# Kernel tuning notes

Measured on AMD Instinct MI355X. Metric: run time of the kernel, lower is better.

## Reference

```python
import jax, jax.numpy as jnp
import numpy as np

D_MODEL = 2048
NUM_EXPERTS = 64
TOP_K = 2


def setup_inputs() -> dict:
    key = jax.random.key(0)
    k_x, k_w = jax.random.split(key)
    x = jax.random.normal(k_x, (4, 8192, D_MODEL), dtype=jnp.float32)
    # nn.Linear(d_model, num_experts, bias=False): weight [num_experts, d_model]
    bound = 1.0 / np.sqrt(D_MODEL)
    W = jax.random.uniform(k_w, (NUM_EXPERTS, D_MODEL), dtype=jnp.float32,
                           minval=-bound, maxval=bound)
    return {"x": x, "W": W}


def reference(x, W):
    # router_logits = x @ W.T : [b, s, num_experts]
    logits = jnp.einsum("bsd,ed->bse", x, W)
    probs = jax.nn.softmax(logits, axis=-1)
    gates, indices = jax.lax.top_k(probs, TOP_K)  # [b, s, top_k]
    gates = gates / jnp.sum(gates, axis=-1, keepdims=True)
    return gates, indices
```

## Files before the change

kernel.cpp:

```cpp
#include <hip/hip_runtime.h>
#include <math.h>
#include <stdint.h>

#define D_MODEL 2048
#define NEXP    64
#define TOKENS  32768
#define BM      128
#define BK      32
#define NT      512
#define NCHUNK  (D_MODEL / BK)
#define BUFSZ   24576
#define TIE_THR 1e-3f
#define LSTRIDE 66

typedef __attribute__((ext_vector_type(8))) short short8;
typedef __attribute__((ext_vector_type(4))) float f32x4;
typedef __attribute__((ext_vector_type(4))) int   i32x4;

typedef __attribute__((address_space(3))) uint32_t       lds_u32_t;
typedef const __attribute__((address_space(1))) uint32_t gbl_u32_t;

__device__ __forceinline__ void split2(float f0, float f1, uint32_t& hw, uint32_t& lw)
{
    const uint32_t u0 = __float_as_uint(f0), u1 = __float_as_uint(f1);
    const uint32_t a0 = u0 & 0xffff0000u, a1 = u1 & 0xffff0000u;
    hw = a1 | (u0 >> 16);
    const float l0 = f0 - __uint_as_float(a0);
    const float l1 = f1 - __uint_as_float(a1);
    lw = (__float_as_uint(l1) & 0xffff0000u) | (__float_as_uint(l0) >> 16);
}

__device__ __forceinline__ void ldsplit(const char* p0, const char* p1,
                                        short8& h8, short8& l8)
{
    const float4 qa = *(const float4*)p0;
    const float4 qb = *(const float4*)p1;
    i32x4 hv, lv;
    uint32_t hw, lw;
    split2(qa.x, qa.y, hw, lw); hv[0] = (int)hw; lv[0] = (int)lw;
    split2(qa.z, qa.w, hw, lw); hv[1] = (int)hw; lv[1] = (int)lw;
    split2(qb.x, qb.y, hw, lw); hv[2] = (int)hw; lv[2] = (int)lw;
    split2(qb.z, qb.w, hw, lw); hv[3] = (int)hw; lv[3] = (int)lw;
    h8 = *(short8*)&hv;
    l8 = *(short8*)&lv;
}

#define WAITVM(N) asm volatile("s_waitcnt vmcnt(" #N ")" ::: "memory")

#define STAGE(c, b)                                                              \
    do {                                                                         \
        char* bb_ = smem + (b) * BUFSZ;                                          \
        __builtin_amdgcn_global_load_lds((gbl_u32_t*)(xsrc0 + (size_t)(c) * BK), \
            (lds_u32_t*)(bb_ + 2048 * wave), 16, 0, 0);                          \
        __builtin_amdgcn_global_load_lds((gbl_u32_t*)(xsrc1 + (size_t)(c) * BK), \
            (lds_u32_t*)(bb_ + 2048 * wave + 1024), 16, 0, 0);                   \
        __builtin_amdgcn_global_load_lds((gbl_u32_t*)(wsrc0 + (size_t)(c) * BK), \
            (lds_u32_t*)(bb_ + 16384 + 1024 * wave), 16, 0, 0);                  \
    } while (0)

#define COMPUTE(b)                                                               \
    do {                                                                         \
        const char* xb_ = smem + (b) * BUFSZ;                                    \
        const char* wb_ = xb_ + 16384;                                           \
        short8 ah_[2], al_[2], bh_[2], bl_[2];                                   \
        _Pragma("unroll")                                                        \
        for (int mi = 0; mi < 2; ++mi)                                           \
            ldsplit(xb_ + oA[mi], xb_ + (oA[mi] ^ 16), ah_[mi], al_[mi]);        \
        _Pragma("unroll")                                                        \
        for (int ni = 0; ni < 2; ++ni)                                           \
            ldsplit(wb_ + oB[ni], wb_ + (oB[ni] ^ 16), bh_[ni], bl_[ni]);        \
        _Pragma("unroll")                                                        \
        for (int mi = 0; mi < 2; ++mi)                                           \
            _Pragma("unroll")                                                    \
            for (int ni = 0; ni < 2; ++ni) {                                     \
                acc[mi][ni] = __builtin_amdgcn_mfma_f32_16x16x32_bf16(ah_[mi], bh_[ni], acc[mi][ni], 0, 0, 0); \
                acc[mi][ni] = __builtin_amdgcn_mfma_f32_16x16x32_bf16(al_[mi], bh_[ni], acc[mi][ni], 0, 0, 0); \
                acc[mi][ni] = __builtin_amdgcn_mfma_f32_16x16x32_bf16(ah_[mi], bl_[ni], acc[mi][ni], 0, 0, 0); \
            }                                                                    \
    } while (0)

__global__ __launch_bounds__(NT, 2)
void router_kernel(const float* __restrict__ x, const float* __restrict__ W,
                   float* __restrict__ out)
{
    __shared__ char smem[4 * BUFSZ];
    __shared__ int  flaglist[BM];
    __shared__ int  nflag;

    const int tid  = threadIdx.x;
    const int lane = tid & 63;
    const int wave = tid >> 6;
    const int row0 = blockIdx.x * BM;

    const int srow = lane >> 3;
    const int scol = 4 * ((lane & 7) ^ srow);
    const float* xsrc0 = x + (size_t)(row0 + 16 * wave + srow) * D_MODEL + scol;
    const float* xsrc1 = x + (size_t)(row0 + 16 * wave + 8 + srow) * D_MODEL + scol;
    const float* wsrc0 = W + (size_t)(8 * wave + srow) * D_MODEL + scol;

    const int fr = lane & 15;
    const int h  = lane >> 4;
    const int m0 = 32 * (wave >> 1);
    const int n0 = 32 * (wave & 1);
    int oA[2], oB[2];
#pragma unroll
    for (int i = 0; i < 2; ++i) {
        oA[i] = (m0 + 16 * i + fr) * 128 + 16 * ((2 * h) ^ (fr & 7));
        oB[i] = (n0 + 16 * i + fr) * 128 + 16 * ((2 * h) ^ (fr & 7));
    }

    f32x4 acc[2][2] = {};

    STAGE(0, 0);
    STAGE(1, 1);
    STAGE(2, 2);

    for (int c = 0; c < NCHUNK - 3; ++c) {
        WAITVM(6);
        __builtin_amdgcn_s_barrier();
        __builtin_amdgcn_sched_barrier(0);
        STAGE(c + 3, (c + 3) & 3);
        COMPUTE(c & 3);
    }
    WAITVM(6); __builtin_amdgcn_s_barrier(); __builtin_amdgcn_sched_barrier(0);
    COMPUTE((NCHUNK - 3) & 3);
    WAITVM(3); __builtin_amdgcn_s_barrier(); __builtin_amdgcn_sched_barrier(0);
    COMPUTE((NCHUNK - 2) & 3);
    WAITVM(0); __builtin_amdgcn_s_barrier(); __builtin_amdgcn_sched_barrier(0);
    COMPUTE((NCHUNK - 1) & 3);
    __syncthreads();

    float* logits = (float*)smem;
#pragma unroll
    for (int mi = 0; mi < 2; ++mi)
#pragma unroll
        for (int ni = 0; ni < 2; ++ni)
#pragma unroll
            for (int r = 0; r < 4; ++r)
                logits[(m0 + 16 * mi + 4 * h + r) * LSTRIDE + n0 + 16 * ni + fr] =
                    acc[mi][ni][r];
    if (tid == 0) nflag = 0;
    __syncthreads();

    float m1 = -INFINITY, m2 = -INFINITY, m3 = -INFINITY;
    int   i1 = 0, i2 = 0;
    bool  tie = false;
    if (tid < BM) {
#pragma unroll 8
        for (int e = 0; e < NEXP; ++e) {
            const float v = logits[tid * LSTRIDE + e];
            if (v > m1)      { m3 = m2; m2 = m1; i2 = i1; m1 = v; i1 = e; }
            else if (v > m2) { m3 = m2; m2 = v; i2 = e; }
            else if (v > m3) { m3 = v; }
        }
        tie = (m1 - m2 < TIE_THR) || (m2 - m3 < TIE_THR);
        if (tie) { const int p = atomicAdd(&nflag, 1); flaglist[p] = tid; }
    }
    __syncthreads();

    const int nf = nflag;
    float* partial = (float*)(smem + 65536);
    for (int f = 0; f < nf; ++f) {
        const int t = flaglist[f];
        const float* xr   = x + (size_t)(row0 + t) * D_MODEL + 256 * wave;
        const float* wrow = W + (size_t)lane * D_MODEL + 256 * wave;
        float ps = 0.f;
        for (int k = 0; k < 256; k += 4) {
            const float4 xv = *(const float4*)(xr + k);
            const float4 wv = *(const float4*)(wrow + k);
            ps = fmaf(xv.x, wv.x, ps); ps = fmaf(xv.y, wv.y, ps);
            ps = fmaf(xv.z, wv.z, ps); ps = fmaf(xv.w, wv.w, ps);
        }
        partial[wave * 64 + lane] = ps;
        __syncthreads();
        if (tid < NEXP) {
            float s = 0.f;
#pragma unroll
            for (int wv = 0; wv < 8; ++wv) s += partial[wv * 64 + tid];
            logits[t * LSTRIDE + tid] = s;
        }
        __syncthreads();
    }

    if (tid < BM) {
        if (tie) {
            m1 = -INFINITY; m2 = -INFINITY; i1 = 0; i2 = 0;
#pragma unroll 8
            for (int e = 0; e < NEXP; ++e) {
                const float v = logits[tid * LSTRIDE + e];
                if (v > m1)      { m2 = m1; i2 = i1; m1 = v; i1 = e; }
                else if (v > m2) { m2 = v; i2 = e; }
            }
        }
        const float ex = expf(m2 - m1);
        const float g1 = 1.0f / (1.0f + ex);
        const float g2 = ex * g1;
        const int row = row0 + tid;
        out[(size_t)row * 2 + 0] = g1;
        out[(size_t)row * 2 + 1] = g2;
        out[(size_t)TOKENS * 2 + (size_t)row * 2 + 0] = (float)i1;
        out[(size_t)TOKENS * 2 + (size_t)row * 2 + 1] = (float)i2;
    }
}

extern "C" void kernel_launch(void* const* d_in, const int* in_sizes, int n_in,
                              void* d_out, int out_size, void* d_ws, size_t ws_size,
                              hipStream_t stream) {
    const float* x = (const float*)d_in[0];
    const float* W = (const float*)d_in[1];
    float* out = (float*)d_out;
    router_kernel<<<TOKENS / BM, NT, 0, stream>>>(x, W, out);
}
```

Measured before the change: 183.6 us.

## Halve row tile to 64 with 4 waves and stagger K-chunk start per block

Each block now handles 64 token rows with 256 threads instead of 128 rows with 512. That doubles the grid and halves LDS per block, which allows more resident blocks and better load balance across CUs. Each wave now stages 16 rows of W instead of 8, so total W traffic doubles. Each block also starts its K loop at a chunk offset derived from its block index, spreading concurrent global reads across different address ranges. The tie-recompute fallback is adjusted to four waves with 512-element slices.

After: 188.2 us. 1.02x slower.

```diff
diff --git a/kernel.cpp b/kernel.cpp
--- a/kernel.cpp
+++ b/kernel.cpp
@@ -5,11 +5,11 @@
 #define D_MODEL 2048
 #define NEXP    64
 #define TOKENS  32768
-#define BM      128
+#define BM      64
 #define BK      32
-#define NT      512
+#define NT      256
 #define NCHUNK  (D_MODEL / BK)
-#define BUFSZ   24576
+#define BUFSZ   16384
 #define TIE_THR 1e-3f
 #define LSTRIDE 66
 
@@ -50,18 +50,21 @@
 #define STAGE(c, b)                                                              \
     do {                                                                         \
         char* bb_ = smem + (b) * BUFSZ;                                          \
-        __builtin_amdgcn_global_load_lds((gbl_u32_t*)(xsrc0 + (size_t)(c) * BK), \
+        const size_t ko_ = (size_t)(c) * BK;                                     \
+        __builtin_amdgcn_global_load_lds((gbl_u32_t*)(xsrc0 + ko_),              \
             (lds_u32_t*)(bb_ + 2048 * wave), 16, 0, 0);                          \
-        __builtin_amdgcn_global_load_lds((gbl_u32_t*)(xsrc1 + (size_t)(c) * BK), \
+        __builtin_amdgcn_global_load_lds((gbl_u32_t*)(xsrc1 + ko_),              \
             (lds_u32_t*)(bb_ + 2048 * wave + 1024), 16, 0, 0);                   \
-        __builtin_amdgcn_global_load_lds((gbl_u32_t*)(wsrc0 + (size_t)(c) * BK), \
-            (lds_u32_t*)(bb_ + 16384 + 1024 * wave), 16, 0, 0);                  \
+        __builtin_amdgcn_global_load_lds((gbl_u32_t*)(wsrc0 + ko_),              \
+            (lds_u32_t*)(bb_ + 8192 + 2048 * wave), 16, 0, 0);                   \
+        __builtin_amdgcn_global_load_lds((gbl_u32_t*)(wsrc1 + ko_),              \
+            (lds_u32_t*)(bb_ + 8192 + 2048 * wave + 1024), 16, 0, 0);            \
     } while (0)
 
 #define COMPUTE(b)                                                               \
     do {                                                                         \
         const char* xb_ = smem + (b) * BUFSZ;                                    \
-        const char* wb_ = xb_ + 16384;                                           \
+        const char* wb_ = xb_ + 8192;                                            \
         short8 ah_[2], al_[2], bh_[2], bl_[2];                                   \
         _Pragma("unroll")                                                        \
         for (int mi = 0; mi < 2; ++mi)                                           \
@@ -91,12 +94,14 @@
     const int lane = tid & 63;
     const int wave = tid >> 6;
     const int row0 = blockIdx.x * BM;
+    const int cstart = blockIdx.x & 63;
 
     const int srow = lane >> 3;
     const int scol = 4 * ((lane & 7) ^ srow);
     const float* xsrc0 = x + (size_t)(row0 + 16 * wave + srow) * D_MODEL + scol;
     const float* xsrc1 = x + (size_t)(row0 + 16 * wave + 8 + srow) * D_MODEL + scol;
-    const float* wsrc0 = W + (size_t)(8 * wave + srow) * D_MODEL + scol;
+    const float* wsrc0 = W + (size_t)(16 * wave + srow) * D_MODEL + scol;
+    const float* wsrc1 = W + (size_t)(16 * wave + 8 + srow) * D_MODEL + scol;
 
     const int fr = lane & 15;
     const int h  = lane >> 4;
@@ -111,20 +116,20 @@
 
     f32x4 acc[2][2] = {};
 
-    STAGE(0, 0);
-    STAGE(1, 1);
-    STAGE(2, 2);
-
-    for (int c = 0; c < NCHUNK - 3; ++c) {
-        WAITVM(6);
+    STAGE((cstart + 0) & 63, 0);
+    STAGE((cstart + 1) & 63, 1);
+    STAGE((cstart + 2) & 63, 2);
+
+    for (int cc = 0; cc < NCHUNK - 3; ++cc) {
+        WAITVM(8);
         __builtin_amdgcn_s_barrier();
         __builtin_amdgcn_sched_barrier(0);
-        STAGE(c + 3, (c + 3) & 3);
-        COMPUTE(c & 3);
-    }
-    WAITVM(6); __builtin_amdgcn_s_barrier(); __builtin_amdgcn_sched_barrier(0);
+        STAGE((cc + 3 + cstart) & 63, (cc + 3) & 3);
+        COMPUTE(cc & 3);
+    }
+    WAITVM(8); __builtin_amdgcn_s_barrier(); __builtin_amdgcn_sched_barrier(0);
     COMPUTE((NCHUNK - 3) & 3);
-    WAITVM(3); __builtin_amdgcn_s_barrier(); __builtin_amdgcn_sched_barrier(0);
+    WAITVM(4); __builtin_amdgcn_s_barrier(); __builtin_amdgcn_sched_barrier(0);
     COMPUTE((NCHUNK - 2) & 3);
     WAITVM(0); __builtin_amdgcn_s_barrier(); __builtin_amdgcn_sched_barrier(0);
     COMPUTE((NCHUNK - 1) & 3);
@@ -159,13 +164,13 @@
     __syncthreads();
 
     const int nf = nflag;
-    float* partial = (float*)(smem + 65536);
+    float* partial = (float*)(smem + 32768);
     for (int f = 0; f < nf; ++f) {
         const int t = flaglist[f];
-        const float* xr   = x + (size_t)(row0 + t) * D_MODEL + 256 * wave;
-        const float* wrow = W + (size_t)lane * D_MODEL + 256 * wave;
+        const float* xr   = x + (size_t)(row0 + t) * D_MODEL + 512 * wave;
+        const float* wrow = W + (size_t)lane * D_MODEL + 512 * wave;
         float ps = 0.f;
-        for (int k = 0; k < 256; k += 4) {
+        for (int k = 0; k < 512; k += 4) {
             const float4 xv = *(const float4*)(xr + k);
             const float4 wv = *(const float4*)(wrow + k);
             ps = fmaf(xv.x, wv.x, ps); ps = fmaf(xv.y, wv.y, ps);
@@ -173,12 +178,9 @@
         }
         partial[wave * 64 + lane] = ps;
         __syncthreads();
-        if (tid < NEXP) {
-            float s = 0.f;
-#pragma unroll
-            for (int wv = 0; wv < 8; ++wv) s += partial[wv * 64 + tid];
-            logits[t * LSTRIDE + tid] = s;
-        }
+        if (tid < NEXP)
+            logits[t * LSTRIDE + tid] = (partial[tid] + partial[64 + tid]) +
+                                        (partial[128 + tid] + partial[192 + tid]);
         __syncthreads();
     }
 
```

## Halve row tile, quadruple K chunk, switch to double-buffered 128KB LDS pipeline

Applied to the files above, without the earlier changes.

Tile changes from 128 rows × 32 K to 64 rows × 128 K per chunk. The pipeline becomes two-stage double buffering in 128KB of LDS, with an extra barrier before each refill. The wave layout and swizzle are reworked so each wave computes 32x16 outputs, and launch bounds drop to one block per CU. The aim is fewer barriers per byte and deeper loads per stage, but it doubles the number of blocks and therefore the re-reads of W, and it lowers occupancy.

Measured after the change: 196.8 us. 7.1% more time.

```diff
diff --git a/kernel.cpp b/kernel.cpp
--- a/kernel.cpp
+++ b/kernel.cpp
@@ -5,11 +5,10 @@
 #define D_MODEL 2048
 #define NEXP    64
 #define TOKENS  32768
-#define BM      128
-#define BK      32
+#define BM      64
+#define BK      128
 #define NT      512
 #define NCHUNK  (D_MODEL / BK)
-#define BUFSZ   24576
 #define TIE_THR 1e-3f
 #define LSTRIDE 66
 
@@ -49,41 +48,46 @@
 
 #define STAGE(c, b)                                                              \
     do {                                                                         \
-        char* bb_ = smem + (b) * BUFSZ;                                          \
-        __builtin_amdgcn_global_load_lds((gbl_u32_t*)(xsrc0 + (size_t)(c) * BK), \
-            (lds_u32_t*)(bb_ + 2048 * wave), 16, 0, 0);                          \
-        __builtin_amdgcn_global_load_lds((gbl_u32_t*)(xsrc1 + (size_t)(c) * BK), \
-            (lds_u32_t*)(bb_ + 2048 * wave + 1024), 16, 0, 0);                   \
-        __builtin_amdgcn_global_load_lds((gbl_u32_t*)(wsrc0 + (size_t)(c) * BK), \
-            (lds_u32_t*)(bb_ + 16384 + 1024 * wave), 16, 0, 0);                  \
+        char* xb_ = smem + (b) * 32768;                                          \
+        char* wb_ = smem + 65536 + (b) * 32768;                                  \
+        const size_t ko_ = (size_t)(c) * (BK * 4);                               \
+        _Pragma("unroll")                                                        \
+        for (int i = 0; i < 4; ++i) {                                            \
+            const int p_ = 4 * wave + i;                                         \
+            __builtin_amdgcn_global_load_lds((gbl_u32_t*)(xsrc[i] + ko_),        \
+                (lds_u32_t*)(xb_ + p_ * 1024), 16, 0, 0);                        \
+            __builtin_amdgcn_global_load_lds((gbl_u32_t*)(wsrc[i] + ko_),        \
+                (lds_u32_t*)(wb_ + p_ * 1024), 16, 0, 0);                        \
+        }                                                                        \
     } while (0)
 
 #define COMPUTE(b)                                                               \
     do {                                                                         \
-        const char* xb_ = smem + (b) * BUFSZ;                                    \
-        const char* wb_ = xb_ + 16384;                                           \
-        short8 ah_[2], al_[2], bh_[2], bl_[2];                                   \
+        const char* xb_ = smem + (b) * 32768;                                    \
+        const char* wb_ = smem + 65536 + (b) * 32768;                            \
         _Pragma("unroll")                                                        \
-        for (int mi = 0; mi < 2; ++mi)                                           \
-            ldsplit(xb_ + oA[mi], xb_ + (oA[mi] ^ 16), ah_[mi], al_[mi]);        \
-        _Pragma("unroll")                                                        \
-        for (int ni = 0; ni < 2; ++ni)                                           \
-            ldsplit(wb_ + oB[ni], wb_ + (oB[ni] ^ 16), bh_[ni], bl_[ni]);        \
-        _Pragma("unroll")                                                        \
-        for (int mi = 0; mi < 2; ++mi)                                           \
+        for (int s = 0; s < 4; ++s) {                                            \
+            const int sq_ = 16 * ((8 * s + 2 * h) ^ key);                        \
+            short8 ah_[2], al_[2], bh_, bl_;                                     \
             _Pragma("unroll")                                                    \
-            for (int ni = 0; ni < 2; ++ni) {                                     \
-                acc[mi][ni] = __builtin_amdgcn_mfma_f32_16x16x32_bf16(ah_[mi], bh_[ni], acc[mi][ni], 0, 0, 0); \
-                acc[mi][ni] = __builtin_amdgcn_mfma_f32_16x16x32_bf16(al_[mi], bh_[ni], acc[mi][ni], 0, 0, 0); \
-                acc[mi][ni] = __builtin_amdgcn_mfma_f32_16x16x32_bf16(ah_[mi], bl_[ni], acc[mi][ni], 0, 0, 0); \
+            for (int mi = 0; mi < 2; ++mi)                                       \
+                ldsplit(xb_ + rowA[mi] + sq_, xb_ + rowA[mi] + sq_ + 16,         \
+                        ah_[mi], al_[mi]);                                       \
+            ldsplit(wb_ + rowB + sq_, wb_ + rowB + sq_ + 16, bh_, bl_);          \
+            _Pragma("unroll")                                                    \
+            for (int mi = 0; mi < 2; ++mi) {                                     \
+                acc[mi] = __builtin_amdgcn_mfma_f32_16x16x32_bf16(ah_[mi], bh_, acc[mi], 0, 0, 0); \
+                acc[mi] = __builtin_amdgcn_mfma_f32_16x16x32_bf16(al_[mi], bh_, acc[mi], 0, 0, 0); \
+                acc[mi] = __builtin_amdgcn_mfma_f32_16x16x32_bf16(ah_[mi], bl_, acc[mi], 0, 0, 0); \
             }                                                                    \
+        }                                                                        \
     } while (0)
 
-__global__ __launch_bounds__(NT, 2)
+__global__ __launch_bounds__(NT, 1)
 void router_kernel(const float* __restrict__ x, const float* __restrict__ W,
                    float* __restrict__ out)
 {
-    __shared__ char smem[4 * BUFSZ];
+    __shared__ char smem[131072];
     __shared__ int  flaglist[BM];
     __shared__ int  nflag;
 
@@ -92,53 +96,53 @@
     const int wave = tid >> 6;
     const int row0 = blockIdx.x * BM;
 
-    const int srow = lane >> 3;
-    const int scol = 4 * ((lane & 7) ^ srow);
-    const float* xsrc0 = x + (size_t)(row0 + 16 * wave + srow) * D_MODEL + scol;
-    const float* xsrc1 = x + (size_t)(row0 + 16 * wave + 8 + srow) * D_MODEL + scol;
-    const float* wsrc0 = W + (size_t)(8 * wave + srow) * D_MODEL + scol;
-
-    const int fr = lane & 15;
-    const int h  = lane >> 4;
-    const int m0 = 32 * (wave >> 1);
-    const int n0 = 32 * (wave & 1);
-    int oA[2], oB[2];
-#pragma unroll
-    for (int i = 0; i < 2; ++i) {
-        oA[i] = (m0 + 16 * i + fr) * 128 + 16 * ((2 * h) ^ (fr & 7));
-        oB[i] = (n0 + 16 * i + fr) * 128 + 16 * ((2 * h) ^ (fr & 7));
-    }
-
-    f32x4 acc[2][2] = {};
+    const int half = lane >> 5;
+    const char* xsrc[4];
+    const char* wsrc[4];
+#pragma unroll
+    for (int i = 0; i < 4; ++i) {
+        const int r = 8 * wave + 2 * i + half;
+        const int q = (lane & 31) ^ (4 * (r & 7));
+        xsrc[i] = (const char*)x + (size_t)(row0 + r) * 8192 + 16 * q;
+        wsrc[i] = (const char*)W + (size_t)r * 8192 + 16 * q;
+    }
+
+    const int fr  = lane & 15;
+    const int h   = lane >> 4;
+    const int m0  = 32 * (wave >> 2);
+    const int n0  = 16 * (wave & 3);
+    const int key = 4 * (fr & 7);
+    int rowA[2];
+#pragma unroll
+    for (int mi = 0; mi < 2; ++mi) rowA[mi] = (m0 + 16 * mi + fr) * 512;
+    const int rowB = (n0 + fr) * 512;
+
+    f32x4 acc[2] = {};
 
     STAGE(0, 0);
     STAGE(1, 1);
-    STAGE(2, 2);
-
-    for (int c = 0; c < NCHUNK - 3; ++c) {
-        WAITVM(6);
+
+    for (int c = 0; c < NCHUNK - 2; ++c) {
+        WAITVM(8);
         __builtin_amdgcn_s_barrier();
         __builtin_amdgcn_sched_barrier(0);
-        STAGE(c + 3, (c + 3) & 3);
-        COMPUTE(c & 3);
-    }
-    WAITVM(6); __builtin_amdgcn_s_barrier(); __builtin_amdgcn_sched_barrier(0);
-    COMPUTE((NCHUNK - 3) & 3);
-    WAITVM(3); __builtin_amdgcn_s_barrier(); __builtin_amdgcn_sched_barrier(0);
-    COMPUTE((NCHUNK - 2) & 3);
+        COMPUTE(c & 1);
+        __builtin_amdgcn_s_barrier();
+        STAGE(c + 2, c & 1);
+    }
+    WAITVM(8); __builtin_amdgcn_s_barrier(); __builtin_amdgcn_sched_barrier(0);
+    COMPUTE((NCHUNK - 2) & 1);
+    __builtin_amdgcn_s_barrier();
     WAITVM(0); __builtin_amdgcn_s_barrier(); __builtin_amdgcn_sched_barrier(0);
-    COMPUTE((NCHUNK - 1) & 3);
+    COMPUTE((NCHUNK - 1) & 1);
     __syncthreads();
 
     float* logits = (float*)smem;
 #pragma unroll
     for (int mi = 0; mi < 2; ++mi)
 #pragma unroll
-        for (int ni = 0; ni < 2; ++ni)
-#pragma unroll
-            for (int r = 0; r < 4; ++r)
-                logits[(m0 + 16 * mi + 4 * h + r) * LSTRIDE + n0 + 16 * ni + fr] =
-                    acc[mi][ni][r];
+        for (int r = 0; r < 4; ++r)
+            logits[(m0 + 16 * mi + 4 * h + r) * LSTRIDE + n0 + fr] = acc[mi][r];
     if (tid == 0) nflag = 0;
     __syncthreads();
 
```
